# Kernel tuning notes

Measured on AMD Instinct MI355X. Metric: run time of the kernel, lower is better.

The kernel has to match this reference:

```python
import jax, jax.numpy as jnp
import numpy as np

B, D, H, A, T = 2048, 512, 512, 18, 16
W_SCALE = 1e-3


def setup_inputs() -> dict:
    key = jax.random.key(0)
    ks = jax.random.split(key, 7)
    xs = jax.random.normal(ks[0], (B, D), dtype=jnp.float32)
    task_id = jax.random.randint(ks[1], (B,), 0, T)
    action = jax.random.randint(ks[2], (B,), 0, A)
    W1 = jax.random.normal(ks[3], (T, D, H), dtype=jnp.float32) * W_SCALE
    b1 = jnp.zeros((T, H), dtype=jnp.float32)
    W2 = jax.random.normal(ks[4], (T, H, A), dtype=jnp.float32) * W_SCALE
    b2 = jnp.zeros((T, A), dtype=jnp.float32)
    return {"xs": xs, "W1": W1, "b1": b1, "W2": W2, "b2": b2,
            "task_id": task_id, "action": action}


def reference(xs, W1, b1, W2, b2, task_id, action):
    # MultiLinear fc1: gather per-sample weight by task_id, batched matmul
    h = jnp.einsum('bd,bdh->bh', xs, W1[task_id]) + b1[task_id]   # [B, H]
    h = jax.nn.relu(h)
    # MultiLinear fc2 -> logits
    logits = jnp.einsum('bh,bha->ba', h, W2[task_id]) + b2[task_id]  # [B, A]
    # Categorical log_prob / entropy
    logp = jax.nn.log_softmax(logits, axis=-1)                       # [B, A]
    log_pi_a = jnp.take_along_axis(logp, action[:, None], axis=-1)   # [B, 1]
    ent = -jnp.sum(jnp.exp(logp) * logp, axis=-1, keepdims=True)     # [B, 1]
    return action, log_pi_a, ent
```

## Files before the change

kernel.cpp:

```cpp
#include <hip/hip_runtime.h>
#include <math.h>

#define B_ 2048
#define D_ 512
#define H_ 512
#define A_ 18
#define T_ 16
#define MTF 16
#define MAXTILESF 144
#define NSLOT 24

typedef __attribute__((ext_vector_type(8))) short short8;
typedef __attribute__((ext_vector_type(4))) float f32x4;

#define W2F_OFF  (3 << 20)
#define W1F_OFF  (4 << 20)
#define WS_NEED  (12 << 20)

__device__ __forceinline__ unsigned short f2bf(float f) {
    union { float f; unsigned int u; } v; v.f = f;
    unsigned int u = v.u;
    return (unsigned short)((u + 0x7fffu + ((u >> 16) & 1u)) >> 16);
}

__global__ __launch_bounds__(256) void nk_prep(const float* __restrict__ W1,
                                               const float* __restrict__ W2,
                                               const int* __restrict__ task_id,
                                               unsigned short* __restrict__ w1f,
                                               unsigned short* __restrict__ w2f,
                                               int* __restrict__ wsi) {
    int bid = blockIdx.x;
    int tid = threadIdx.x;
    if (bid < 1024) {
        __shared__ float tile[64][65];
        int hx = bid & 7, dy = (bid >> 3) & 7, t = bid >> 6;
        const float* src = W1 + ((size_t)t * D_ + dy * 64) * H_ + hx * 64;
        int f4 = tid & 15, ry = tid >> 4;
#pragma unroll
        for (int i = 0; i < 4; ++i) {
            int row = ry + i * 16;
            float4 v = *(const float4*)(src + (size_t)row * H_ + f4 * 4);
            tile[row][f4 * 4 + 0] = v.x;
            tile[row][f4 * 4 + 1] = v.y;
            tile[row][f4 * 4 + 2] = v.z;
            tile[row][f4 * 4 + 3] = v.w;
        }
        __syncthreads();
#pragma unroll
        for (int j = 0; j < 2; ++j) {
            int cch = tid * 2 + j;
            int ntl = cch >> 7;
            int ksl = (cch >> 6) & 1;
            int ln = cch & 63;
            int rr = ln & 15, kk = ln >> 4;
            unsigned short uu[8];
#pragma unroll
            for (int i = 0; i < 8; ++i)
                uu[i] = f2bf(tile[ksl * 32 + kk * 8 + i][ntl * 16 + rr]);
            size_t dst = (((size_t)t * 32 + hx * 4 + ntl) * 16 + dy * 2 + ksl) * 512
                         + (size_t)ln * 8;
            *(uint4*)(w1f + dst) = *(const uint4*)uu;
        }
    } else if (bid < 1040) {
        int t = bid - 1024;
        const float* src = W2 + (size_t)t * H_ * A_;
#pragma unroll
        for (int j = 0; j < 8; ++j) {
            int cch = tid * 8 + j;
            int atl = cch >> 10;
            int ks = (cch >> 6) & 15;
            int ln = cch & 63;
            int rr = ln & 15, kk = ln >> 4;
            int a = atl * 16 + rr;
            unsigned short uu[8];
#pragma unroll
            for (int i = 0; i < 8; ++i) {
                int h = ks * 32 + kk * 8 + i;
                uu[i] = (a < A_) ? f2bf(src[(size_t)h * A_ + a]) : (unsigned short)0;
            }
            size_t dst = (((size_t)t * 2 + atl) * 16 + ks) * 512 + (size_t)ln * 8;
            *(uint4*)(w2f + dst) = *(const uint4*)uu;
        }
    } else {
        __shared__ int cnt[T_], cur[T_], soff[T_];
        if (tid < T_) { cnt[tid] = 0; cur[tid] = 0; }
        __syncthreads();
        for (int b = tid; b < B_; b += 256) atomicAdd(&cnt[task_id[b]], 1);
        __syncthreads();
        if (tid == 0) {
            int off = 0;
            for (int t = 0; t < T_; ++t) {
                soff[t] = off; wsi[17 + t] = off;
                off += cnt[t];
            }
            wsi[17 + T_] = off;
        }
        __syncthreads();
        for (int b = tid; b < B_; b += 256) {
            int t = task_id[b];
            int pos = atomicAdd(&cur[t], 1);
            wsi[256 + soff[t] + pos] = b;
        }
    }
}

__global__ __launch_bounds__(512) void nk_fused(
        const float* __restrict__ xs,
        const unsigned short* __restrict__ w1f,
        const unsigned short* __restrict__ w2f,
        const float* __restrict__ b1, const float* __restrict__ b2,
        const int* __restrict__ action, float* __restrict__ out,
        const int* __restrict__ wsi) {
    __shared__ unsigned short x_lds[16][520];
    __shared__ unsigned short h_lds[16][520];
    __shared__ float lg_lds[16][34];
    __shared__ int sidx[16];

    int c = blockIdx.x;
    int tid = threadIdx.x, lane = tid & 63, w = tid >> 6;
    int r15 = lane & 15, kg = lane >> 4;

    int o0 = wsi[17 + c],     n0 = wsi[18 + c] - o0;
    int o1 = wsi[17 + c + 8], n1 = wsi[18 + c + 8] - o1;
    int nt0 = (n0 + 15) >> 4, nt1 = (n1 + 15) >> 4;
    int ntot = nt0 + nt1;

    for (int u = blockIdx.y; u < ntot; u += NSLOT) {
        int t, kt, off0, rT;
        if (u < nt0) { t = c; kt = u; off0 = o0; rT = n0; }
        else { t = c + 8; kt = u - nt0; off0 = o1; rT = n1; }
        int rowbase = off0 + kt * 16;
        int rows = rT - kt * 16; if (rows > 16) rows = 16;

        if (tid < 16) sidx[tid] = wsi[256 + rowbase + (tid < rows ? tid : rows - 1)];
        __syncthreads();

        {
            int row = tid >> 5, col = (tid & 31) * 16;
            const float* src = xs + (size_t)sidx[row] * D_ + col;
            float4 v0 = *(const float4*)(src);
            float4 v1 = *(const float4*)(src + 4);
            float4 v2 = *(const float4*)(src + 8);
            float4 v3 = *(const float4*)(src + 12);
            unsigned short uu[16] = {
                f2bf(v0.x), f2bf(v0.y), f2bf(v0.z), f2bf(v0.w),
                f2bf(v1.x), f2bf(v1.y), f2bf(v1.z), f2bf(v1.w),
                f2bf(v2.x), f2bf(v2.y), f2bf(v2.z), f2bf(v2.w),
                f2bf(v3.x), f2bf(v3.y), f2bf(v3.z), f2bf(v3.w) };
            *(uint4*)&x_lds[row][col]     = *(const uint4*)&uu[0];
            *(uint4*)&x_lds[row][col + 8] = *(const uint4*)&uu[8];
        }
        __syncthreads();

        const unsigned short* bw = w1f + ((size_t)t * 32 + w * 4) * 16 * 512
                                   + (size_t)lane * 8;
        f32x4 acc0 = {0.f,0.f,0.f,0.f}, acc1 = {0.f,0.f,0.f,0.f};
        f32x4 acc2 = {0.f,0.f,0.f,0.f}, acc3 = {0.f,0.f,0.f,0.f};
#pragma unroll
        for (int ks = 0; ks < 16; ++ks) {
            short8 af = *(const short8*)&x_lds[r15][ks * 32 + kg * 8];
            short8 b0 = *(const short8*)(bw + (size_t)(0 * 16 + ks) * 512);
            short8 b1f = *(const short8*)(bw + (size_t)(1 * 16 + ks) * 512);
            short8 b2f = *(const short8*)(bw + (size_t)(2 * 16 + ks) * 512);
            short8 b3f = *(const short8*)(bw + (size_t)(3 * 16 + ks) * 512);
            acc0 = __builtin_amdgcn_mfma_f32_16x16x32_bf16(af, b0, acc0, 0, 0, 0);
            acc1 = __builtin_amdgcn_mfma_f32_16x16x32_bf16(af, b1f, acc1, 0, 0, 0);
            acc2 = __builtin_amdgcn_mfma_f32_16x16x32_bf16(af, b2f, acc2, 0, 0, 0);
            acc3 = __builtin_amdgcn_mfma_f32_16x16x32_bf16(af, b3f, acc3, 0, 0, 0);
        }

        int colb = w * 64 + r15;
        float bv0 = b1[t * H_ + colb];
        float bv1 = b1[t * H_ + colb + 16];
        float bv2 = b1[t * H_ + colb + 32];
        float bv3 = b1[t * H_ + colb + 48];
#pragma unroll
        for (int j = 0; j < 4; ++j) {
            int row = kg * 4 + j;
            float v;
            v = acc0[j] + bv0; h_lds[row][colb]      = f2bf(v > 0.f ? v : 0.f);
            v = acc1[j] + bv1; h_lds[row][colb + 16] = f2bf(v > 0.f ? v : 0.f);
            v = acc2[j] + bv2; h_lds[row][colb + 32] = f2bf(v > 0.f ? v : 0.f);
            v = acc3[j] + bv3; h_lds[row][colb + 48] = f2bf(v > 0.f ? v : 0.f);
        }
        __syncthreads();

        if (w < 2) {
            const unsigned short* wa = w2f + ((size_t)t * 2 + w) * 16 * 512
                                       + (size_t)lane * 8;
            f32x4 c0 = {0.f,0.f,0.f,0.f};
#pragma unroll
            for (int ks = 0; ks < 16; ++ks) {
                short8 hf = *(const short8*)&h_lds[r15][ks * 32 + kg * 8];
                short8 w0 = *(const short8*)(wa + (size_t)ks * 512);
                c0 = __builtin_amdgcn_mfma_f32_16x16x32_bf16(hf, w0, c0, 0, 0, 0);
            }
            int a = w * 16 + r15;
            float bb = (a < A_) ? b2[t * A_ + a] : 0.f;
#pragma unroll
            for (int j = 0; j < 4; ++j) {
                lg_lds[kg * 4 + j][a] = c0[j] + bb;
            }
        }
        __syncthreads();

        if (tid < rows) {
            int b = sidx[tid];
            float logits[A_];
            float m = -1e30f;
#pragma unroll
            for (int a = 0; a < A_; ++a) {
                logits[a] = lg_lds[tid][a];
                m = fmaxf(m, logits[a]);
            }
            float S = 0.f, sle = 0.f;
#pragma unroll
            for (int a = 0; a < A_; ++a) {
                float e = expf(logits[a] - m);
                S += e;
                sle += logits[a] * e;
            }
            float logZ = m + logf(S);
            int as = action[b];
            out[b] = (float)as;
            out[B_ + b] = logits[as] - logZ;
            out[2 * B_ + b] = logZ - sle / S;
        }
        __syncthreads();
    }
}


__global__ void nk_init(int* wsi) { int i = threadIdx.x; if (i < 50) wsi[i] = 0; }

__global__ void nk_count(const int* task_id, int* wsi) {
    int b = blockIdx.x * blockDim.x + threadIdx.x;
    if (b < B_) atomicAdd(&wsi[1 + task_id[b]], 1);
}

__global__ void nk_plan(int* wsi) {
    int off = 0, tot = 0;
    for (int t = 0; t < T_; ++t) {
        wsi[17 + t] = off;
        int cnt = wsi[1 + t];
        int nt = (cnt + MTF - 1) / MTF;
        for (int k = 0; k < nt; ++k) wsi[50 + tot++] = (t << 16) | k;
        off += cnt;
    }
    wsi[17 + T_] = off;
    wsi[0] = tot;
}

__global__ void nk_scatter(const int* task_id, int* wsi) {
    int b = blockIdx.x * blockDim.x + threadIdx.x;
    if (b < B_) {
        int t = task_id[b];
        int pos = atomicAdd(&wsi[34 + t], 1);
        wsi[256 + wsi[17 + t] + pos] = b;
    }
}

__global__ __launch_bounds__(512) void nk_main(
        const float* __restrict__ xs, const float* __restrict__ W1,
        const float* __restrict__ b1, const float* __restrict__ W2,
        const float* __restrict__ b2, const int* __restrict__ task_id,
        const int* __restrict__ action, float* __restrict__ out,
        const int* __restrict__ wsi) {
    __shared__ float tile[MTF][D_];
    __shared__ int sidx[MTF];
    int bid = blockIdx.x;
    if (bid >= wsi[0]) return;
    int code = wsi[50 + bid];
    int t = code >> 16, kt = code & 0xffff;
    int off0 = wsi[17 + t], off1 = wsi[17 + t + 1];
    int base = off0 + kt * MTF;
    int rows = off1 - base; if (rows > MTF) rows = MTF;
    int tid = threadIdx.x;
    if (tid < MTF) sidx[tid] = (tid < rows) ? wsi[256 + base + tid] : -1;
    __syncthreads();
    for (int i = 0; i < MTF; ++i) {
        int b = sidx[i];
        tile[i][tid] = (b >= 0) ? xs[(size_t)b * D_ + tid] : 0.f;
    }
    __syncthreads();
    const float* w1p = W1 + (size_t)t * D_ * H_ + tid;
    float acc[MTF];
#pragma unroll
    for (int i = 0; i < MTF; ++i) acc[i] = 0.f;
    for (int d = 0; d < D_; d += 4) {
        float w0 = w1p[(size_t)(d + 0) * H_];
        float w1v = w1p[(size_t)(d + 1) * H_];
        float w2v = w1p[(size_t)(d + 2) * H_];
        float w3v = w1p[(size_t)(d + 3) * H_];
#pragma unroll
        for (int i = 0; i < MTF; ++i) {
            float4 x = *(const float4*)&tile[i][d];
            float a0 = fmaf(x.x, w0, acc[i]);
            a0 = fmaf(x.y, w1v, a0);
            a0 = fmaf(x.z, w2v, a0);
            acc[i] = fmaf(x.w, w3v, a0);
        }
    }
    __syncthreads();
    float b1v = b1[t * H_ + tid];
#pragma unroll
    for (int i = 0; i < MTF; ++i) {
        float h = acc[i] + b1v;
        tile[i][tid] = h > 0.f ? h : 0.f;
    }
    __syncthreads();
    int g = tid >> 5, l = tid & 31;
    float lg[A_];
#pragma unroll
    for (int a = 0; a < A_; ++a) lg[a] = 0.f;
    const float* w2base = W2 + (size_t)t * H_ * A_;
    for (int hh = l; hh < H_; hh += 32) {
        float hv = tile[g][hh];
        const float* wrow = w2base + (size_t)hh * A_;
#pragma unroll
        for (int a = 0; a < A_; ++a) lg[a] = fmaf(hv, wrow[a], lg[a]);
    }
#pragma unroll
    for (int a = 0; a < A_; ++a) {
        lg[a] += __shfl_down(lg[a], 16, 32);
        lg[a] += __shfl_down(lg[a], 8, 32);
        lg[a] += __shfl_down(lg[a], 4, 32);
        lg[a] += __shfl_down(lg[a], 2, 32);
        lg[a] += __shfl_down(lg[a], 1, 32);
    }
    if (l == 0 && g < rows) {
        int b = sidx[g];
        float logits[A_];
        float m = -1e30f;
#pragma unroll
        for (int a = 0; a < A_; ++a) {
            logits[a] = lg[a] + b2[t * A_ + a];
            m = fmaxf(m, logits[a]);
        }
        float S = 0.f, sle = 0.f;
#pragma unroll
        for (int a = 0; a < A_; ++a) {
            float e = expf(logits[a] - m);
            S += e;
            sle += logits[a] * e;
        }
        float logZ = m + logf(S);
        int as = action[b];
        out[b] = (float)as;
        out[B_ + b] = logits[as] - logZ;
        out[2 * B_ + b] = logZ - sle / S;
    }
}

extern "C" void kernel_launch(void* const* d_in, const int* in_sizes, int n_in,
                              void* d_out, int out_size, void* d_ws, size_t ws_size,
                              hipStream_t stream) {
    const float* xs = (const float*)d_in[0];
    const float* W1 = (const float*)d_in[1];
    const float* b1 = (const float*)d_in[2];
    const float* W2 = (const float*)d_in[3];
    const float* b2 = (const float*)d_in[4];
    const int* task_id = (const int*)d_in[5];
    const int* action = (const int*)d_in[6];
    float* out = (float*)d_out;

    if (ws_size >= WS_NEED) {
        unsigned char* wsb = (unsigned char*)d_ws;
        int* wsi = (int*)d_ws;
        unsigned short* w2f = (unsigned short*)(wsb + W2F_OFF);
        unsigned short* w1f = (unsigned short*)(wsb + W1F_OFF);

        nk_prep<<<1041, 256, 0, stream>>>(W1, W2, task_id, w1f, w2f, wsi);
        nk_fused<<<dim3(8, NSLOT), 512, 0, stream>>>(xs, w1f, w2f, b1, b2,
                                                     action, out, wsi);
    } else {
        int* wsi = (int*)d_ws;
        nk_init<<<1, 64, 0, stream>>>(wsi);
        nk_count<<<(B_ + 255) / 256, 256, 0, stream>>>(task_id, wsi);
        nk_plan<<<1, 1, 0, stream>>>(wsi);
        nk_scatter<<<(B_ + 255) / 256, 256, 0, stream>>>(task_id, wsi);
        nk_main<<<MAXTILESF, 512, 0, stream>>>(xs, W1, b1, W2, b2, task_id, action, out, wsi);
    }
}
```

Measured before the change: 31.93 us.

## Split fc1 across H quarters with register-resident weights and separate softmax pass

The fused kernel is restructured so each block owns one task, one quarter of the hidden dimension and half of that task's row tiles. Its W1 and W2 fragments are loaded once into registers and reused across all its row tiles, instead of being re-streamed from global memory for every tile. Partial fc2 logits per H-quarter go to a workspace buffer, and a new final kernel sums them, adds b2 and computes log-softmax and entropy. xs is also converted to bf16 in the prep kernel. In exchange, the change adds a kernel launch, partial-sum global traffic and heavier register pressure from 16 short8 fragments per lane.

```diff
diff --git a/kernel.cpp b/kernel.cpp
--- a/kernel.cpp
+++ b/kernel.cpp
@@ -8,14 +8,15 @@
 #define T_ 16
 #define MTF 16
 #define MAXTILESF 144
-#define NSLOT 24
 
 typedef __attribute__((ext_vector_type(8))) short short8;
 typedef __attribute__((ext_vector_type(4))) float f32x4;
 
-#define W2F_OFF  (3 << 20)
-#define W1F_OFF  (4 << 20)
-#define WS_NEED  (12 << 20)
+#define PART_OFF 16384
+#define XSB_OFF  (2 << 20)
+#define W2F_OFF  (4 << 20)
+#define W1F_OFF  (5 << 20)
+#define WS_NEED  (13 << 20)
 
 __device__ __forceinline__ unsigned short f2bf(float f) {
     union { float f; unsigned int u; } v; v.f = f;
@@ -24,9 +25,11 @@
 }
 
 __global__ __launch_bounds__(256) void nk_prep(const float* __restrict__ W1,
+                                               const float* __restrict__ xs,
                                                const float* __restrict__ W2,
                                                const int* __restrict__ task_id,
                                                unsigned short* __restrict__ w1f,
+                                               unsigned short* __restrict__ xs_b,
                                                unsigned short* __restrict__ w2f,
                                                int* __restrict__ wsi) {
     int bid = blockIdx.x;
@@ -61,8 +64,15 @@
                          + (size_t)ln * 8;
             *(uint4*)(w1f + dst) = *(const uint4*)uu;
         }
-    } else if (bid < 1040) {
-        int t = bid - 1024;
+    } else if (bid < 1536) {
+        size_t off = ((size_t)(bid - 1024) * 256 + tid) * 8;
+        float4 x0 = *(const float4*)(xs + off);
+        float4 x1 = *(const float4*)(xs + off + 4);
+        unsigned short uu[8] = { f2bf(x0.x), f2bf(x0.y), f2bf(x0.z), f2bf(x0.w),
+                                 f2bf(x1.x), f2bf(x1.y), f2bf(x1.z), f2bf(x1.w) };
+        *(uint4*)(xs_b + off) = *(const uint4*)uu;
+    } else if (bid < 1552) {
+        int t = bid - 1536;
         const float* src = W2 + (size_t)t * H_ * A_;
 #pragma unroll
         for (int j = 0; j < 8; ++j) {
@@ -104,130 +114,138 @@
     }
 }
 
-__global__ __launch_bounds__(512) void nk_fused(
-        const float* __restrict__ xs,
+__global__ __launch_bounds__(512) void nk_gemm(
+        const unsigned short* __restrict__ xs_b,
         const unsigned short* __restrict__ w1f,
         const unsigned short* __restrict__ w2f,
-        const float* __restrict__ b1, const float* __restrict__ b2,
-        const int* __restrict__ action, float* __restrict__ out,
+        const float* __restrict__ b1,
+        float* __restrict__ part,
         const int* __restrict__ wsi) {
     __shared__ unsigned short x_lds[16][520];
-    __shared__ unsigned short h_lds[16][520];
-    __shared__ float lg_lds[16][34];
+    __shared__ unsigned short h_lds[16][136];
     __shared__ int sidx[16];
 
     int c = blockIdx.x;
+    int s = blockIdx.y;
+    int t = c + ((s >> 2) & 1) * 8;
+    int cq = s & 3;
+    int mh = s >> 3;
+
+    int o = wsi[17 + t];
+    int n = wsi[18 + t] - o;
+
     int tid = threadIdx.x, lane = tid & 63, w = tid >> 6;
     int r15 = lane & 15, kg = lane >> 4;
 
-    int o0 = wsi[17 + c],     n0 = wsi[18 + c] - o0;
-    int o1 = wsi[17 + c + 8], n1 = wsi[18 + c + 8] - o1;
-    int nt0 = (n0 + 15) >> 4, nt1 = (n1 + 15) >> 4;
-    int ntot = nt0 + nt1;
-
-    for (int u = blockIdx.y; u < ntot; u += NSLOT) {
-        int t, kt, off0, rT;
-        if (u < nt0) { t = c; kt = u; off0 = o0; rT = n0; }
-        else { t = c + 8; kt = u - nt0; off0 = o1; rT = n1; }
-        int rowbase = off0 + kt * 16;
-        int rows = rT - kt * 16; if (rows > 16) rows = 16;
+    const unsigned short* bw = w1f + ((size_t)t * 32 + cq * 8 + w) * 16 * 512
+                               + (size_t)lane * 8;
+    short8 breg[16];
+#pragma unroll
+    for (int ks = 0; ks < 16; ++ks)
+        breg[ks] = *(const short8*)(bw + (size_t)ks * 512);
+
+    int wa_sel = (w < 2) ? w : 0;
+    const unsigned short* wa = w2f + ((size_t)t * 2 + wa_sel) * 16 * 512
+                               + (size_t)lane * 8;
+    short8 w2frag[4];
+#pragma unroll
+    for (int j = 0; j < 4; ++j)
+        w2frag[j] = *(const short8*)(wa + (size_t)(cq * 4 + j) * 512);
+
+    float bv = b1[t * H_ + cq * 128 + w * 16 + r15];
+
+    int nmt = (n + 15) >> 4;
+    int half = (nmt + 1) >> 1;
+    int m0 = mh * half;
+    int m1 = m0 + half; if (m1 > nmt) m1 = nmt;
+
+    for (int mt = m0; mt < m1; ++mt) {
+        int rowbase = o + mt * 16;
+        int rows = n - mt * 16; if (rows > 16) rows = 16;
 
         if (tid < 16) sidx[tid] = wsi[256 + rowbase + (tid < rows ? tid : rows - 1)];
         __syncthreads();
 
         {
             int row = tid >> 5, col = (tid & 31) * 16;
-            const float* src = xs + (size_t)sidx[row] * D_ + col;
-            float4 v0 = *(const float4*)(src);
-            float4 v1 = *(const float4*)(src + 4);
-            float4 v2 = *(const float4*)(src + 8);
-            float4 v3 = *(const float4*)(src + 12);
-            unsigned short uu[16] = {
-                f2bf(v0.x), f2bf(v0.y), f2bf(v0.z), f2bf(v0.w),
-                f2bf(v1.x), f2bf(v1.y), f2bf(v1.z), f2bf(v1.w),
-                f2bf(v2.x), f2bf(v2.y), f2bf(v2.z), f2bf(v2.w),
-                f2bf(v3.x), f2bf(v3.y), f2bf(v3.z), f2bf(v3.w) };
-            *(uint4*)&x_lds[row][col]     = *(const uint4*)&uu[0];
-            *(uint4*)&x_lds[row][col + 8] = *(const uint4*)&uu[8];
-        }
-        __syncthreads();
-
-        const unsigned short* bw = w1f + ((size_t)t * 32 + w * 4) * 16 * 512
-                                   + (size_t)lane * 8;
-        f32x4 acc0 = {0.f,0.f,0.f,0.f}, acc1 = {0.f,0.f,0.f,0.f};
-        f32x4 acc2 = {0.f,0.f,0.f,0.f}, acc3 = {0.f,0.f,0.f,0.f};
-#pragma unroll
-        for (int ks = 0; ks < 16; ++ks) {
-            short8 af = *(const short8*)&x_lds[r15][ks * 32 + kg * 8];
-            short8 b0 = *(const short8*)(bw + (size_t)(0 * 16 + ks) * 512);
-            short8 b1f = *(const short8*)(bw + (size_t)(1 * 16 + ks) * 512);
-            short8 b2f = *(const short8*)(bw + (size_t)(2 * 16 + ks) * 512);
-            short8 b3f = *(const short8*)(bw + (size_t)(3 * 16 + ks) * 512);
-            acc0 = __builtin_amdgcn_mfma_f32_16x16x32_bf16(af, b0, acc0, 0, 0, 0);
-            acc1 = __builtin_amdgcn_mfma_f32_16x16x32_bf16(af, b1f, acc1, 0, 0, 0);
-            acc2 = __builtin_amdgcn_mfma_f32_16x16x32_bf16(af, b2f, acc2, 0, 0, 0);
-            acc3 = __builtin_amdgcn_mfma_f32_16x16x32_bf16(af, b3f, acc3, 0, 0, 0);
-        }
-
-        int colb = w * 64 + r15;
-        float bv0 = b1[t * H_ + colb];
-        float bv1 = b1[t * H_ + colb + 16];
-        float bv2 = b1[t * H_ + colb + 32];
-        float bv3 = b1[t * H_ + colb + 48];
+            const unsigned short* src = xs_b + (size_t)sidx[row] * D_ + col;
+            uint4 v0 = *(const uint4*)(src);
+            uint4 v1 = *(const uint4*)(src + 8);
+            *(uint4*)&x_lds[row][col] = v0;
+            *(uint4*)&x_lds[row][col + 8] = v1;
+        }
+        __syncthreads();
+
+        f32x4 accA = {0.f,0.f,0.f,0.f}, accB = {0.f,0.f,0.f,0.f};
+#pragma unroll
+        for (int ks = 0; ks < 16; ks += 2) {
+            short8 a0 = *(const short8*)&x_lds[r15][ks * 32 + kg * 8];
+            short8 a1 = *(const short8*)&x_lds[r15][(ks + 1) * 32 + kg * 8];
+            accA = __builtin_amdgcn_mfma_f32_16x16x32_bf16(a0, breg[ks], accA, 0, 0, 0);
+            accB = __builtin_amdgcn_mfma_f32_16x16x32_bf16(a1, breg[ks + 1], accB, 0, 0, 0);
+        }
+
 #pragma unroll
         for (int j = 0; j < 4; ++j) {
-            int row = kg * 4 + j;
-            float v;
-            v = acc0[j] + bv0; h_lds[row][colb]      = f2bf(v > 0.f ? v : 0.f);
-            v = acc1[j] + bv1; h_lds[row][colb + 16] = f2bf(v > 0.f ? v : 0.f);
-            v = acc2[j] + bv2; h_lds[row][colb + 32] = f2bf(v > 0.f ? v : 0.f);
-            v = acc3[j] + bv3; h_lds[row][colb + 48] = f2bf(v > 0.f ? v : 0.f);
+            float v = accA[j] + accB[j] + bv;
+            h_lds[kg * 4 + j][w * 16 + r15] = f2bf(v > 0.f ? v : 0.f);
         }
         __syncthreads();
 
         if (w < 2) {
-            const unsigned short* wa = w2f + ((size_t)t * 2 + w) * 16 * 512
-                                       + (size_t)lane * 8;
-            f32x4 c0 = {0.f,0.f,0.f,0.f};
-#pragma unroll
-            for (int ks = 0; ks < 16; ++ks) {
-                short8 hf = *(const short8*)&h_lds[r15][ks * 32 + kg * 8];
-                short8 w0 = *(const short8*)(wa + (size_t)ks * 512);
-                c0 = __builtin_amdgcn_mfma_f32_16x16x32_bf16(hf, w0, c0, 0, 0, 0);
+            f32x4 p = {0.f,0.f,0.f,0.f};
+#pragma unroll
+            for (int j = 0; j < 4; ++j) {
+                short8 hf = *(const short8*)&h_lds[r15][j * 32 + kg * 8];
+                p = __builtin_amdgcn_mfma_f32_16x16x32_bf16(hf, w2frag[j], p, 0, 0, 0);
             }
-            int a = w * 16 + r15;
-            float bb = (a < A_) ? b2[t * A_ + a] : 0.f;
 #pragma unroll
             for (int j = 0; j < 4; ++j) {
-                lg_lds[kg * 4 + j][a] = c0[j] + bb;
+                int lr = kg * 4 + j;
+                if (lr < rows)
+                    part[((size_t)cq * B_ + rowbase + lr) * 32 + w * 16 + r15] = p[j];
             }
         }
         __syncthreads();
-
-        if (tid < rows) {
-            int b = sidx[tid];
-            float logits[A_];
-            float m = -1e30f;
-#pragma unroll
-            for (int a = 0; a < A_; ++a) {
-                logits[a] = lg_lds[tid][a];
-                m = fmaxf(m, logits[a]);
-            }
-            float S = 0.f, sle = 0.f;
-#pragma unroll
-            for (int a = 0; a < A_; ++a) {
-                float e = expf(logits[a] - m);
-                S += e;
-                sle += logits[a] * e;
-            }
-            float logZ = m + logf(S);
-            int as = action[b];
-            out[b] = (float)as;
-            out[B_ + b] = logits[as] - logZ;
-            out[2 * B_ + b] = logZ - sle / S;
-        }
-        __syncthreads();
-    }
+    }
+}
+
+__global__ __launch_bounds__(256) void nk_final(const float* __restrict__ part,
+                                                const float* __restrict__ b2,
+                                                const int* __restrict__ action,
+                                                float* __restrict__ out,
+                                                const int* __restrict__ wsi) {
+    int r = blockIdx.x * 256 + threadIdx.x;
+    if (r >= B_) return;
+    int t = 0;
+#pragma unroll
+    for (int i = 1; i < T_; ++i) t += (r >= wsi[17 + i]) ? 1 : 0;
+    int b = wsi[256 + r];
+
+    float logits[A_];
+#pragma unroll
+    for (int a = 0; a < A_; ++a) logits[a] = b2[t * A_ + a];
+#pragma unroll
+    for (int cq = 0; cq < 4; ++cq) {
+        const float* pc = part + ((size_t)cq * B_ + r) * 32;
+#pragma unroll
+        for (int a = 0; a < A_; ++a) logits[a] += pc[a];
+    }
+    float m = -1e30f;
+#pragma unroll
+    for (int a = 0; a < A_; ++a) m = fmaxf(m, logits[a]);
+    float S = 0.f, sle = 0.f;
+#pragma unroll
+    for (int a = 0; a < A_; ++a) {
+        float e = expf(logits[a] - m);
+        S += e;
+        sle += logits[a] * e;
+    }
+    float logZ = m + logf(S);
+    int as = action[b];
+    out[b] = (float)as;
+    out[B_ + b] = logits[as] - logZ;
+    out[2 * B_ + b] = logZ - sle / S;
 }
 
 
@@ -367,12 +385,14 @@
     if (ws_size >= WS_NEED) {
         unsigned char* wsb = (unsigned char*)d_ws;
         int* wsi = (int*)d_ws;
+        float* part = (float*)(wsb + PART_OFF);
+        unsigned short* xs_b = (unsigned short*)(wsb + XSB_OFF);
         unsigned short* w2f = (unsigned short*)(wsb + W2F_OFF);
         unsigned short* w1f = (unsigned short*)(wsb + W1F_OFF);
 
-        nk_prep<<<1041, 256, 0, stream>>>(W1, W2, task_id, w1f, w2f, wsi);
-        nk_fused<<<dim3(8, NSLOT), 512, 0, stream>>>(xs, w1f, w2f, b1, b2,
-                                                     action, out, wsi);
+        nk_prep<<<1553, 256, 0, stream>>>(W1, xs, W2, task_id, w1f, xs_b, w2f, wsi);
+        nk_gemm<<<dim3(8, 16), 512, 0, stream>>>(xs_b, w1f, w2f, b1, part, wsi);
+        nk_final<<<(B_ + 255) / 256, 256, 0, stream>>>(part, b2, action, out, wsi);
     } else {
         int* wsi = (int*)d_ws;
         nk_init<<<1, 64, 0, stream>>>(wsi);
```

Result: slower. 41.12 us (+28.8%).

## Split hidden dimension across blocks and finish softmax in separate kernel

Applied to the files above, without the earlier changes.

Each 16-row tile is now split into two halves of the hidden dimension (256 columns each), doubling the number of work units and raising the grid's y-dimension from 24 to 40 slots. Each half computes partial logits and writes them to a workspace buffer. A new nk_final kernel sums the two partials, adds b2, and computes the log-softmax outputs. The goal is more parallelism and less per-block work, at the cost of recomputing the x tile load per half, extra global traffic for the partials, and an additional kernel launch.

```diff
diff --git a/kernel.cpp b/kernel.cpp
--- a/kernel.cpp
+++ b/kernel.cpp
@@ -8,11 +8,12 @@
 #define T_ 16
 #define MTF 16
 #define MAXTILESF 144
-#define NSLOT 24
+#define NSLOT 40
 
 typedef __attribute__((ext_vector_type(8))) short short8;
 typedef __attribute__((ext_vector_type(4))) float f32x4;
 
+#define PART_OFF 16384
 #define W2F_OFF  (3 << 20)
 #define W1F_OFF  (4 << 20)
 #define WS_NEED  (12 << 20)
@@ -108,12 +109,11 @@
         const float* __restrict__ xs,
         const unsigned short* __restrict__ w1f,
         const unsigned short* __restrict__ w2f,
-        const float* __restrict__ b1, const float* __restrict__ b2,
-        const int* __restrict__ action, float* __restrict__ out,
+        const float* __restrict__ b1,
+        float* __restrict__ part,
         const int* __restrict__ wsi) {
     __shared__ unsigned short x_lds[16][520];
-    __shared__ unsigned short h_lds[16][520];
-    __shared__ float lg_lds[16][34];
+    __shared__ unsigned short h_lds[16][264];
     __shared__ int sidx[16];
 
     int c = blockIdx.x;
@@ -123,12 +123,13 @@
     int o0 = wsi[17 + c],     n0 = wsi[18 + c] - o0;
     int o1 = wsi[17 + c + 8], n1 = wsi[18 + c + 8] - o1;
     int nt0 = (n0 + 15) >> 4, nt1 = (n1 + 15) >> 4;
-    int ntot = nt0 + nt1;
+    int ntot = (nt0 + nt1) * 2;
 
     for (int u = blockIdx.y; u < ntot; u += NSLOT) {
+        int uu2 = u >> 1, ch = u & 1;
         int t, kt, off0, rT;
-        if (u < nt0) { t = c; kt = u; off0 = o0; rT = n0; }
-        else { t = c + 8; kt = u - nt0; off0 = o1; rT = n1; }
+        if (uu2 < nt0) { t = c; kt = uu2; off0 = o0; rT = n0; }
+        else { t = c + 8; kt = uu2 - nt0; off0 = o1; rT = n1; }
         int rowbase = off0 + kt * 16;
         int rows = rT - kt * 16; if (rows > 16) rows = 16;
 
@@ -142,92 +143,97 @@
             float4 v1 = *(const float4*)(src + 4);
             float4 v2 = *(const float4*)(src + 8);
             float4 v3 = *(const float4*)(src + 12);
-            unsigned short uu[16] = {
+            unsigned short uu8[16] = {
                 f2bf(v0.x), f2bf(v0.y), f2bf(v0.z), f2bf(v0.w),
                 f2bf(v1.x), f2bf(v1.y), f2bf(v1.z), f2bf(v1.w),
                 f2bf(v2.x), f2bf(v2.y), f2bf(v2.z), f2bf(v2.w),
                 f2bf(v3.x), f2bf(v3.y), f2bf(v3.z), f2bf(v3.w) };
-            *(uint4*)&x_lds[row][col]     = *(const uint4*)&uu[0];
-            *(uint4*)&x_lds[row][col + 8] = *(const uint4*)&uu[8];
-        }
-        __syncthreads();
-
-        const unsigned short* bw = w1f + ((size_t)t * 32 + w * 4) * 16 * 512
+            *(uint4*)&x_lds[row][col]     = *(const uint4*)&uu8[0];
+            *(uint4*)&x_lds[row][col + 8] = *(const uint4*)&uu8[8];
+        }
+        __syncthreads();
+
+        const unsigned short* bw = w1f + ((size_t)t * 32 + ch * 16 + w * 2) * 16 * 512
                                    + (size_t)lane * 8;
         f32x4 acc0 = {0.f,0.f,0.f,0.f}, acc1 = {0.f,0.f,0.f,0.f};
-        f32x4 acc2 = {0.f,0.f,0.f,0.f}, acc3 = {0.f,0.f,0.f,0.f};
 #pragma unroll
         for (int ks = 0; ks < 16; ++ks) {
             short8 af = *(const short8*)&x_lds[r15][ks * 32 + kg * 8];
             short8 b0 = *(const short8*)(bw + (size_t)(0 * 16 + ks) * 512);
             short8 b1f = *(const short8*)(bw + (size_t)(1 * 16 + ks) * 512);
-            short8 b2f = *(const short8*)(bw + (size_t)(2 * 16 + ks) * 512);
-            short8 b3f = *(const short8*)(bw + (size_t)(3 * 16 + ks) * 512);
             acc0 = __builtin_amdgcn_mfma_f32_16x16x32_bf16(af, b0, acc0, 0, 0, 0);
             acc1 = __builtin_amdgcn_mfma_f32_16x16x32_bf16(af, b1f, acc1, 0, 0, 0);
-            acc2 = __builtin_amdgcn_mfma_f32_16x16x32_bf16(af, b2f, acc2, 0, 0, 0);
-            acc3 = __builtin_amdgcn_mfma_f32_16x16x32_bf16(af, b3f, acc3, 0, 0, 0);
-        }
-
-        int colb = w * 64 + r15;
-        float bv0 = b1[t * H_ + colb];
-        float bv1 = b1[t * H_ + colb + 16];
-        float bv2 = b1[t * H_ + colb + 32];
-        float bv3 = b1[t * H_ + colb + 48];
+        }
+
+        int colg = ch * 256 + w * 32 + r15;
+        float bv0 = b1[t * H_ + colg];
+        float bv1 = b1[t * H_ + colg + 16];
 #pragma unroll
         for (int j = 0; j < 4; ++j) {
             int row = kg * 4 + j;
             float v;
-            v = acc0[j] + bv0; h_lds[row][colb]      = f2bf(v > 0.f ? v : 0.f);
-            v = acc1[j] + bv1; h_lds[row][colb + 16] = f2bf(v > 0.f ? v : 0.f);
-            v = acc2[j] + bv2; h_lds[row][colb + 32] = f2bf(v > 0.f ? v : 0.f);
-            v = acc3[j] + bv3; h_lds[row][colb + 48] = f2bf(v > 0.f ? v : 0.f);
+            v = acc0[j] + bv0; h_lds[row][w * 32 + r15]      = f2bf(v > 0.f ? v : 0.f);
+            v = acc1[j] + bv1; h_lds[row][w * 32 + 16 + r15] = f2bf(v > 0.f ? v : 0.f);
         }
         __syncthreads();
 
         if (w < 2) {
             const unsigned short* wa = w2f + ((size_t)t * 2 + w) * 16 * 512
                                        + (size_t)lane * 8;
-            f32x4 c0 = {0.f,0.f,0.f,0.f};
-#pragma unroll
-            for (int ks = 0; ks < 16; ++ks) {
-                short8 hf = *(const short8*)&h_lds[r15][ks * 32 + kg * 8];
-                short8 w0 = *(const short8*)(wa + (size_t)ks * 512);
-                c0 = __builtin_amdgcn_mfma_f32_16x16x32_bf16(hf, w0, c0, 0, 0, 0);
+            f32x4 p = {0.f,0.f,0.f,0.f};
+#pragma unroll
+            for (int j = 0; j < 8; ++j) {
+                short8 hf = *(const short8*)&h_lds[r15][j * 32 + kg * 8];
+                short8 wf = *(const short8*)(wa + (size_t)(ch * 8 + j) * 512);
+                p = __builtin_amdgcn_mfma_f32_16x16x32_bf16(hf, wf, p, 0, 0, 0);
             }
-            int a = w * 16 + r15;
-            float bb = (a < A_) ? b2[t * A_ + a] : 0.f;
 #pragma unroll
             for (int j = 0; j < 4; ++j) {
-                lg_lds[kg * 4 + j][a] = c0[j] + bb;
+                int lr = kg * 4 + j;
+                if (lr < rows)
+                    part[((size_t)ch * B_ + rowbase + lr) * 32 + w * 16 + r15] = p[j];
             }
         }
         __syncthreads();
-
-        if (tid < rows) {
-            int b = sidx[tid];
-            float logits[A_];
-            float m = -1e30f;
-#pragma unroll
-            for (int a = 0; a < A_; ++a) {
-                logits[a] = lg_lds[tid][a];
-                m = fmaxf(m, logits[a]);
-            }
-            float S = 0.f, sle = 0.f;
-#pragma unroll
-            for (int a = 0; a < A_; ++a) {
-                float e = expf(logits[a] - m);
-                S += e;
-                sle += logits[a] * e;
-            }
-            float logZ = m + logf(S);
-            int as = action[b];
-            out[b] = (float)as;
-            out[B_ + b] = logits[as] - logZ;
-            out[2 * B_ + b] = logZ - sle / S;
-        }
-        __syncthreads();
-    }
+    }
+}
+
+__global__ __launch_bounds__(256) void nk_final(const float* __restrict__ part,
+                                                const float* __restrict__ b2,
+                                                const int* __restrict__ action,
+                                                float* __restrict__ out,
+                                                const int* __restrict__ wsi) {
+    int r = blockIdx.x * 256 + threadIdx.x;
+    if (r >= B_) return;
+    int t = 0;
+#pragma unroll
+    for (int i = 1; i < T_; ++i) t += (r >= wsi[17 + i]) ? 1 : 0;
+    int b = wsi[256 + r];
+
+    float logits[A_];
+#pragma unroll
+    for (int a = 0; a < A_; ++a) logits[a] = b2[t * A_ + a];
+#pragma unroll
+    for (int ch = 0; ch < 2; ++ch) {
+        const float* pc = part + ((size_t)ch * B_ + r) * 32;
+#pragma unroll
+        for (int a = 0; a < A_; ++a) logits[a] += pc[a];
+    }
+    float m = -1e30f;
+#pragma unroll
+    for (int a = 0; a < A_; ++a) m = fmaxf(m, logits[a]);
+    float S = 0.f, sle = 0.f;
+#pragma unroll
+    for (int a = 0; a < A_; ++a) {
+        float e = expf(logits[a] - m);
+        S += e;
+        sle += logits[a] * e;
+    }
+    float logZ = m + logf(S);
+    int as = action[b];
+    out[b] = (float)as;
+    out[B_ + b] = logits[as] - logZ;
+    out[2 * B_ + b] = logZ - sle / S;
 }
 
 
@@ -367,12 +373,13 @@
     if (ws_size >= WS_NEED) {
         unsigned char* wsb = (unsigned char*)d_ws;
         int* wsi = (int*)d_ws;
+        float* part = (float*)(wsb + PART_OFF);
         unsigned short* w2f = (unsigned short*)(wsb + W2F_OFF);
         unsigned short* w1f = (unsigned short*)(wsb + W1F_OFF);
 
         nk_prep<<<1041, 256, 0, stream>>>(W1, W2, task_id, w1f, w2f, wsi);
-        nk_fused<<<dim3(8, NSLOT), 512, 0, stream>>>(xs, w1f, w2f, b1, b2,
-                                                     action, out, wsi);
+        nk_fused<<<dim3(8, NSLOT), 512, 0, stream>>>(xs, w1f, w2f, b1, part, wsi);
+        nk_final<<<(B_ + 255) / 256, 256, 0, stream>>>(part, b2, action, out, wsi);
     } else {
         int* wsi = (int*)d_ws;
         nk_init<<<1, 64, 0, stream>>>(wsi);
```

Result: slower. 34.23 us (+7.2%).
